# Kernel optimization log

Measured on AMD Instinct MI355X. Metric: run time of the kernel, lower is better.

The kernel has to match this reference:

```python
import jax, jax.numpy as jnp
import numpy as np

NUM_USERS = 50000
NUM_ITEMS = 50000
EMBED_DIM = 128
NUM_LAYERS = 3
NUM_EDGES = 600000
N_NODES = NUM_USERS + NUM_ITEMS


def setup_inputs() -> dict:
    key = jax.random.key(0)
    k1, k2, k3, k4, k5 = jax.random.split(key, 5)
    edge_index = jax.random.randint(k1, (2, NUM_EDGES), 0, N_NODES, dtype=jnp.int64 if jax.config.x64_enabled else jnp.int32)
    user_emb = jax.random.normal(k2, (NUM_USERS, EMBED_DIM), jnp.float32) * 0.1
    item_emb = jax.random.normal(k3, (NUM_ITEMS, EMBED_DIM), jnp.float32) * 0.1
    Wa = jax.random.normal(k4, (NUM_LAYERS, 2 * EMBED_DIM, 1), jnp.float32) * 0.05
    ba = jnp.zeros((NUM_LAYERS, 1), jnp.float32)
    Wg = jax.random.normal(k5, (NUM_LAYERS, 2 * EMBED_DIM, EMBED_DIM), jnp.float32) * 0.05
    bg = jnp.zeros((NUM_LAYERS, EMBED_DIM), jnp.float32)
    return {"edge_index": edge_index, "user_emb": user_emb, "item_emb": item_emb,
            "Wa": Wa, "ba": ba, "Wg": Wg, "bg": bg}


def reference(edge_index, user_emb, item_emb, Wa, ba, Wg, bg):
    U = user_emb.shape[0]
    N = U + item_emb.shape[0]
    src, dst = edge_index[0], edge_index[1]
    x = jnp.concatenate([user_emb, item_emb], axis=0)  # [N, d]
    for l in range(Wa.shape[0]):
        src_emb = x[src]                                # [E, d] gather
        dst_emb = x[dst]                                # [E, d] gather
        cat = jnp.concatenate([src_emb, dst_emb], 1)    # [E, 2d]
        att = jax.nn.sigmoid(cat @ Wa[l] + ba[l])       # [E, 1]
        # attention-weighted scatter-sum over destination node (zeros for isolated nodes)
        agg = jax.ops.segment_sum(src_emb * att, dst, num_segments=N)  # [N, d]
        x = jax.nn.relu(jnp.concatenate([x, agg], 1) @ Wg[l] + bg[l])  # [N, d]
    return x[:U], x[U:]
```

## Files before the change

kernel.cpp:

```cpp
#include <hip/hip_runtime.h>
#include <cstddef>
#include <cstdint>

#define NUSERS 50000
#define NITEMS 50000
#define NNODES 100000
#define DIM    128
#define NLAYERS 3
#define NEDGES 600000
#define NPAD 100096

#define EBLK  8192
#define NBLK  74
#define NBUCK 782

#define PRO_CONCAT 6250
#define PRO_WG     48
#define PRO_TOTAL  (PRO_CONCAT + PRO_WG + NBLK)

typedef __attribute__((ext_vector_type(8))) short short8;
typedef __attribute__((ext_vector_type(4))) float f32x4;

__device__ __forceinline__ float bf_lo(unsigned u) { return __uint_as_float(u << 16); }
__device__ __forceinline__ float bf_hi(unsigned u) { return __uint_as_float(u & 0xffff0000u); }
__device__ __forceinline__ unsigned short f2bf(float f) {
    unsigned b = __float_as_uint(f);
    return (unsigned short)((b + 0x7fffu + ((b >> 16) & 1u)) >> 16);
}

__device__ __forceinline__ void async16(const void* g, void* l) {
    __builtin_amdgcn_global_load_lds(
        (const __attribute__((address_space(1))) unsigned int*)(uintptr_t)g,
        (__attribute__((address_space(3))) unsigned int*)(unsigned int)(uintptr_t)l,
        16, 0, 0);
}

__global__ __launch_bounds__(256) void prologue_kernel(
        const float* __restrict__ ue, const float* __restrict__ ie,
        const float* __restrict__ Wa, const float* __restrict__ ba,
        const float* __restrict__ Wg, const int* __restrict__ dst,
        unsigned short* __restrict__ xb,
        float* __restrict__ a_src, float* __restrict__ a_dst,
        unsigned short* __restrict__ Bf, unsigned* __restrict__ counts) {
    __shared__ unsigned hist[NBUCK];
    const int blk = blockIdx.x;

    if (blk < PRO_CONCAT) {
        const int n = blk * 16 + (threadIdx.x >> 4);
        if (n >= NNODES) return;
        const int sub = threadIdx.x & 15;
        const float* r = (n < NUSERS) ? (ue + (size_t)n * DIM)
                                      : (ie + (size_t)(n - NUSERS) * DIM);
        const float4 v0 = *(const float4*)(r + sub * 8);
        const float4 v1 = *(const float4*)(r + sub * 8 + 4);
        const float4 wl0 = *(const float4*)(Wa + sub * 8);
        const float4 wl1 = *(const float4*)(Wa + sub * 8 + 4);
        const float4 wh0 = *(const float4*)(Wa + DIM + sub * 8);
        const float4 wh1 = *(const float4*)(Wa + DIM + sub * 8 + 4);

        uint4 o;
        o.x = ((unsigned)f2bf(v0.y) << 16) | (unsigned)f2bf(v0.x);
        o.y = ((unsigned)f2bf(v0.w) << 16) | (unsigned)f2bf(v0.z);
        o.z = ((unsigned)f2bf(v1.y) << 16) | (unsigned)f2bf(v1.x);
        o.w = ((unsigned)f2bf(v1.w) << 16) | (unsigned)f2bf(v1.z);
        *(uint4*)(xb + (size_t)n * DIM + sub * 8) = o;

        float ps = v0.x * wl0.x + v0.y * wl0.y + v0.z * wl0.z + v0.w * wl0.w
                 + v1.x * wl1.x + v1.y * wl1.y + v1.z * wl1.z + v1.w * wl1.w;
        float pd = v0.x * wh0.x + v0.y * wh0.y + v0.z * wh0.z + v0.w * wh0.w
                 + v1.x * wh1.x + v1.y * wh1.y + v1.z * wh1.z + v1.w * wh1.w;
        #pragma unroll
        for (int off = 1; off < 16; off <<= 1) {
            ps += __shfl_xor(ps, off);
            pd += __shfl_xor(pd, off);
        }
        if (sub == 0) { a_src[n] = ps; a_dst[n] = pd + ba[0]; }
    } else if (blk < PRO_CONCAT + PRO_WG) {
        const int tid = (blk - PRO_CONCAT) * 256 + threadIdx.x;
        if (tid >= NLAYERS * 4096) return;
        const int l    = tid >> 12;
        const int slot = tid & 4095;
        const int lane = slot & 63;
        const int t2   = slot >> 6;
        const int nf   = t2 & 3;
        const int t3   = t2 >> 2;
        const int ks   = t3 & 7;
        const int nb   = t3 >> 3;
        const int col  = nb * 64 + nf * 16 + (lane & 15);
        const int k0   = ks * 32 + (lane >> 4) * 8;
        const float* wsrc = Wg + (size_t)l * 256 * DIM;
        unsigned short o[8];
        #pragma unroll
        for (int j = 0; j < 8; ++j) o[j] = f2bf(wsrc[(size_t)(k0 + j) * DIM + col]);
        *(short8*)(Bf + (size_t)tid * 8) = *(short8*)o;
    } else {
        const int bblk = blk - PRO_CONCAT - PRO_WG;
        for (int i = threadIdx.x; i < NBUCK; i += 256) hist[i] = 0;
        __syncthreads();
        const int base = bblk * EBLK;
        const int end  = (base + EBLK < NEDGES) ? base + EBLK : NEDGES;
        for (int e = base + threadIdx.x; e < end; e += 256)
            atomicAdd(&hist[dst[e] >> 7], 1u);
        __syncthreads();
        for (int i = threadIdx.x; i < NBUCK; i += 256)
            counts[(size_t)bblk * NBUCK + i] = hist[i];
    }
}

__global__ __launch_bounds__(1024) void prefix_kernel(
        unsigned* __restrict__ counts, unsigned* __restrict__ bucketbase) {
    const int b = threadIdx.x;
    unsigned tot = 0;
    if (b < NBUCK) {
        for (int i = 0; i < NBLK; ++i) {
            const unsigned c = counts[(size_t)i * NBUCK + b];
            counts[(size_t)i * NBUCK + b] = tot;
            tot += c;
        }
    }
    const int lane = b & 63, w = b >> 6;
    unsigned s = tot;
    #pragma unroll
    for (int o = 1; o < 64; o <<= 1) {
        unsigned t = (unsigned)__shfl_up((int)s, o);
        if (lane >= o) s += t;
    }
    __shared__ unsigned wsum[16];
    if (lane == 63) wsum[w] = s;
    __syncthreads();
    unsigned add = 0;
    #pragma unroll
    for (int j = 0; j < 15; ++j) if (w > j) add += wsum[j];
    if (b < NBUCK) bucketbase[b] = s + add - tot;
    if (b == NBUCK - 1) bucketbase[NBUCK] = s + add;
}

__global__ __launch_bounds__(256) void bin_scatter_kernel(
        const int* __restrict__ src, const int* __restrict__ dst,
        const unsigned* __restrict__ counts, const unsigned* __restrict__ bucketbase,
        unsigned* __restrict__ pairs) {
    __shared__ unsigned off[NBUCK];
    for (int i = threadIdx.x; i < NBUCK; i += 256)
        off[i] = bucketbase[i] + counts[(size_t)blockIdx.x * NBUCK + i];
    __syncthreads();
    const int base = blockIdx.x * EBLK;
    const int end  = (base + EBLK < NEDGES) ? base + EBLK : NEDGES;
    for (int e = base + threadIdx.x; e < end; e += 256) {
        const int d = dst[e];
        const unsigned pos = atomicAdd(&off[d >> 7], 1u);
        pairs[pos] = ((unsigned)(d & 127) << 17) | (unsigned)src[e];
    }
}

__global__ __launch_bounds__(256) void bucket_csr_kernel(
        const unsigned* __restrict__ pairs, const unsigned* __restrict__ bucketbase,
        int* __restrict__ row_start, int* __restrict__ csr_src) {
    __shared__ unsigned deg[128], rs[128], fill[128];
    const int b = blockIdx.x;
    const unsigned seg0 = bucketbase[b], seg1 = bucketbase[b + 1];
    const int t = threadIdx.x;
    if (t < 128) deg[t] = 0;
    __syncthreads();
    for (unsigned i = seg0 + t; i < seg1; i += 256)
        atomicAdd(&deg[pairs[i] >> 17], 1u);
    __syncthreads();
    if (t < 128) rs[t] = deg[t];
    __syncthreads();
    #pragma unroll
    for (int o = 1; o < 128; o <<= 1) {
        unsigned tmp = 0;
        if (t < 128 && t >= o) tmp = rs[t - o];
        __syncthreads();
        if (t < 128) rs[t] += tmp;
        __syncthreads();
    }
    if (t < 128) {
        const unsigned excl = rs[t] - deg[t];
        fill[t] = excl;
        const int node = b * 128 + t;
        if (node < NNODES) row_start[node] = (int)(seg0 + excl);
    }
    __syncthreads();
    for (unsigned i = seg0 + t; i < seg1; i += 256) {
        const unsigned p = pairs[i];
        const unsigned r = atomicAdd(&fill[p >> 17], 1u);
        csr_src[seg0 + r] = (int)(p & 0x1ffffu);
    }
    if (b == 0 && t == 0) row_start[NNODES] = NEDGES;
}

__global__ __launch_bounds__(256) void pull_agg_kernel(
        const int* __restrict__ row_start, const int* __restrict__ csr_src,
        const float* __restrict__ a_src, const float* __restrict__ a_dst,
        const unsigned short* __restrict__ xb, unsigned short* __restrict__ aggb) {
    const int n = blockIdx.x * 16 + (threadIdx.x >> 4);
    if (n >= NNODES) return;
    const int lane = threadIdx.x & 63;
    const int sub  = lane & 15;
    const int qb   = lane & 48;
    const int beg = row_start[n], end = row_start[n + 1];
    const float adst = a_dst[n];

    float a0 = 0, a1 = 0, a2 = 0, a3 = 0, a4 = 0, a5 = 0, a6 = 0, a7 = 0;

    for (int base = beg; base < end; base += 16) {
        const int rem = end - base;
        const int cnt = rem < 16 ? rem : 16;
        int   idx_l = 0;
        float att_l = 0.0f;
        if (sub < cnt) {
            idx_l = csr_src[base + sub];
            att_l = 1.0f / (1.0f + __expf(-(a_src[idx_l] + adst)));
        }
        int i = 0;
        for (; i + 3 < cnt; i += 4) {
            const int   s0 = __shfl(idx_l, qb + i);
            const int   s1 = __shfl(idx_l, qb + i + 1);
            const int   s2 = __shfl(idx_l, qb + i + 2);
            const int   s3 = __shfl(idx_l, qb + i + 3);
            const float w0 = __shfl(att_l, qb + i);
            const float w1 = __shfl(att_l, qb + i + 1);
            const float w2 = __shfl(att_l, qb + i + 2);
            const float w3 = __shfl(att_l, qb + i + 3);
            const uint4 u0 = *(const uint4*)(xb + (size_t)s0 * DIM + sub * 8);
            const uint4 u1 = *(const uint4*)(xb + (size_t)s1 * DIM + sub * 8);
            const uint4 u2 = *(const uint4*)(xb + (size_t)s2 * DIM + sub * 8);
            const uint4 u3 = *(const uint4*)(xb + (size_t)s3 * DIM + sub * 8);
            a0 += bf_lo(u0.x) * w0 + bf_lo(u1.x) * w1 + bf_lo(u2.x) * w2 + bf_lo(u3.x) * w3;
            a1 += bf_hi(u0.x) * w0 + bf_hi(u1.x) * w1 + bf_hi(u2.x) * w2 + bf_hi(u3.x) * w3;
            a2 += bf_lo(u0.y) * w0 + bf_lo(u1.y) * w1 + bf_lo(u2.y) * w2 + bf_lo(u3.y) * w3;
            a3 += bf_hi(u0.y) * w0 + bf_hi(u1.y) * w1 + bf_hi(u2.y) * w2 + bf_hi(u3.y) * w3;
            a4 += bf_lo(u0.z) * w0 + bf_lo(u1.z) * w1 + bf_lo(u2.z) * w2 + bf_lo(u3.z) * w3;
            a5 += bf_hi(u0.z) * w0 + bf_hi(u1.z) * w1 + bf_hi(u2.z) * w2 + bf_hi(u3.z) * w3;
            a6 += bf_lo(u0.w) * w0 + bf_lo(u1.w) * w1 + bf_lo(u2.w) * w2 + bf_lo(u3.w) * w3;
            a7 += bf_hi(u0.w) * w0 + bf_hi(u1.w) * w1 + bf_hi(u2.w) * w2 + bf_hi(u3.w) * w3;
        }
        for (; i < cnt; ++i) {
            const int   s = __shfl(idx_l, qb + i);
            const float w = __shfl(att_l, qb + i);
            const uint4 u = *(const uint4*)(xb + (size_t)s * DIM + sub * 8);
            a0 += bf_lo(u.x) * w;  a1 += bf_hi(u.x) * w;
            a2 += bf_lo(u.y) * w;  a3 += bf_hi(u.y) * w;
            a4 += bf_lo(u.z) * w;  a5 += bf_hi(u.z) * w;
            a6 += bf_lo(u.w) * w;  a7 += bf_hi(u.w) * w;
        }
    }

    uint4 o;
    o.x = ((unsigned)f2bf(a1) << 16) | (unsigned)f2bf(a0);
    o.y = ((unsigned)f2bf(a3) << 16) | (unsigned)f2bf(a2);
    o.z = ((unsigned)f2bf(a5) << 16) | (unsigned)f2bf(a4);
    o.w = ((unsigned)f2bf(a7) << 16) | (unsigned)f2bf(a6);
    *(uint4*)(aggb + (size_t)n * DIM + sub * 8) = o;
}

__global__ __launch_bounds__(256, 7) void gemm_mfma_kernel(
        unsigned short* __restrict__ xb, const unsigned short* __restrict__ aggb,
        const unsigned short* __restrict__ bfr, const float* __restrict__ bg,
        const float* __restrict__ wa_next, const float* __restrict__ ba_next,
        float* __restrict__ a_src, float* __restrict__ a_dst,
        float* __restrict__ xout_f32, int write_f32, int do_dots) {
    __shared__ unsigned short At[2][32 * 128];
    __shared__ float psS[4][32], psD[4][32];

    const int tid  = threadIdx.x;
    const int lane = tid & 63;
    const int wid  = tid >> 6;
    const int mbase = blockIdx.x * 32;

    #pragma unroll
    for (int h = 0; h < 2; ++h) {
        const unsigned short* s = h ? aggb : xb;
        #pragma unroll
        for (int i = 0; i < 2; ++i) {
            const int lrow = i * 16 + wid * 4 + (lane >> 4);
            const int c    = (lane & 15) ^ (lrow & 7);
            async16(s + (size_t)(mbase + lrow) * DIM + c * 8,
                    &At[h][(i * 16 + wid * 4) * 128]);
        }
    }

    const int l16 = lane & 15, kq = lane >> 4;
    const unsigned short* bfw = bfr + (size_t)(wid >> 1) * (8 * 4 * 64 * 8);
    const int nfo = (wid & 1) * 2;

    f32x4 acc[2][2] = {};

    asm volatile("s_waitcnt vmcnt(2)" ::: "memory");
    __builtin_amdgcn_s_barrier();

    #pragma unroll
    for (int ks = 0; ks < 8; ++ks) {
        if (ks == 4) {
            asm volatile("s_waitcnt vmcnt(0)" ::: "memory");
            __builtin_amdgcn_s_barrier();
        }
        const int h = ks >> 2, ksl = ks & 3;
        short8 b[2], a[2];
        #pragma unroll
        for (int nf = 0; nf < 2; ++nf)
            b[nf] = *(const short8*)(bfw + ((size_t)(ks * 4 + nfo + nf) * 64 + lane) * 8);
        #pragma unroll
        for (int mf = 0; mf < 2; ++mf) {
            const int row   = mf * 16 + l16;
            const int chunk = (ksl * 4 + kq) ^ (row & 7);
            a[mf] = *(const short8*)&At[h][row * 128 + chunk * 8];
        }
        #pragma unroll
        for (int mf = 0; mf < 2; ++mf)
            #pragma unroll
            for (int nf = 0; nf < 2; ++nf)
                acc[mf][nf] = __builtin_amdgcn_mfma_f32_16x16x32_bf16(
                    a[mf], b[nf], acc[mf][nf], 0, 0, 0);
    }

    const int rsub = kq * 4;
    float waS[2] = {0, 0}, waD[2] = {0, 0}, bias[2];
    #pragma unroll
    for (int nf = 0; nf < 2; ++nf) {
        const int col = wid * 32 + nf * 16 + l16;
        bias[nf] = bg[col];
        if (do_dots) { waS[nf] = wa_next[col]; waD[nf] = wa_next[DIM + col]; }
    }
    #pragma unroll
    for (int mf = 0; mf < 2; ++mf) {
        #pragma unroll
        for (int j = 0; j < 4; ++j) {
            const int row = mbase + mf * 16 + rsub + j;
            float s = 0.0f, d = 0.0f;
            #pragma unroll
            for (int nf = 0; nf < 2; ++nf) {
                const int col = wid * 32 + nf * 16 + l16;
                const float v = fmaxf(acc[mf][nf][j] + bias[nf], 0.0f);
                if (write_f32) {
                    xout_f32[(size_t)row * DIM + col] = v;
                } else {
                    const unsigned short bv = f2bf(v);
                    const unsigned pb = (unsigned)(unsigned short)__shfl_xor((int)bv, 1);
                    if (!(l16 & 1))
                        *(unsigned*)(xb + (size_t)row * DIM + col) =
                            (unsigned)bv | (pb << 16);
                }
                s += v * waS[nf];
                d += v * waD[nf];
            }
            if (do_dots) {
                #pragma unroll
                for (int off = 1; off < 16; off <<= 1) {
                    s += __shfl_xor(s, off);
                    d += __shfl_xor(d, off);
                }
                if (l16 == 0) {
                    const int rl = mf * 16 + rsub + j;
                    psS[wid][rl] = s;
                    psD[wid][rl] = d;
                }
            }
        }
    }
    if (do_dots) {
        __syncthreads();
        if (tid < 32) {
            const int row = mbase + tid;
            a_src[row] = psS[0][tid] + psS[1][tid] + psS[2][tid] + psS[3][tid];
            a_dst[row] = psD[0][tid] + psD[1][tid] + psD[2][tid] + psD[3][tid]
                       + ba_next[0];
        }
    }
}

extern "C" void kernel_launch(void* const* d_in, const int* in_sizes, int n_in,
                              void* d_out, int out_size, void* d_ws, size_t ws_size,
                              hipStream_t stream) {
    const int*   edge = (const int*)d_in[0];
    const float* ue   = (const float*)d_in[1];
    const float* ie   = (const float*)d_in[2];
    const float* Wa   = (const float*)d_in[3];
    const float* ba   = (const float*)d_in[4];
    const float* Wg   = (const float*)d_in[5];
    const float* bg   = (const float*)d_in[6];

    const int* src = edge;
    const int* dst = edge + NEDGES;

    float* x = (float*)d_out;

    unsigned short* xb   = (unsigned short*)d_ws;
    unsigned short* aggb = xb + (size_t)NPAD * DIM;
    unsigned short* bfr  = aggb + (size_t)NPAD * DIM;
    float* a_src      = (float*)(bfr + NLAYERS * 32768);
    float* a_dst      = a_src + NPAD;
    int*   row_start  = (int*)(a_dst + NPAD);
    int*   csr_src    = row_start + NPAD + 256;
    unsigned* pairs   = (unsigned*)(csr_src + NEDGES);
    unsigned* counts  = pairs + NEDGES;
    unsigned* bbase   = counts + (size_t)NBLK * NBUCK;

    prologue_kernel<<<PRO_TOTAL, 256, 0, stream>>>(
        ue, ie, Wa, ba, Wg, dst, xb, a_src, a_dst, bfr, counts);

    prefix_kernel<<<1, 1024, 0, stream>>>(counts, bbase);
    bin_scatter_kernel<<<NBLK, 256, 0, stream>>>(src, dst, counts, bbase, pairs);
    bucket_csr_kernel<<<NBUCK, 256, 0, stream>>>(pairs, bbase, row_start, csr_src);

    const int gemm_blocks = NNODES / 32;
    const int pull_blocks = (NNODES + 15) / 16;
    for (int l = 0; l < NLAYERS; ++l) {
        pull_agg_kernel<<<pull_blocks, 256, 0, stream>>>(
            row_start, csr_src, a_src, a_dst, xb, aggb);
        const int last = (l == NLAYERS - 1);
        gemm_mfma_kernel<<<gemm_blocks, 256, 0, stream>>>(
            xb, aggb, bfr + (size_t)l * 32768, bg + (size_t)l * DIM,
            Wa + (size_t)(l + 1 < NLAYERS ? l + 1 : 0) * 256,
            ba + (l + 1 < NLAYERS ? l + 1 : 0),
            a_src, a_dst, x, last ? 1 : 0, last ? 0 : 1);
    }
}
```

Baseline: 222.8 us.

## Use 8 lanes per node in pull aggregation and transpose bucket counts

The pull aggregation kernel now assigns 8 lanes per destination node, each handling 16 features with two 16-byte loads, so each wave covers 8 nodes and processes neighbor chunks of 8. The aim is to cut idle lanes on low-degree nodes (average degree is about 6) and raise memory-level parallelism. The per-block bucket counts are stored transposed with padding, so the prefix scan reads contiguous rows. The bucket CSR scan switches from a shared-memory Hillis-Steele loop with many barriers to wave shuffles. The per-thread register footprint of the pull kernel grows, and the bounds check is dropped because 100000 divides evenly by 32.

Result: slower. 261.5 us (+17.3%).

```diff
diff --git a/kernel.cpp b/kernel.cpp
--- a/kernel.cpp
+++ b/kernel.cpp
@@ -12,6 +12,7 @@
 
 #define EBLK  8192
 #define NBLK  74
+#define NBLKP 76
 #define NBUCK 782
 
 #define PRO_CONCAT 6250
@@ -26,6 +27,9 @@
 __device__ __forceinline__ unsigned short f2bf(float f) {
     unsigned b = __float_as_uint(f);
     return (unsigned short)((b + 0x7fffu + ((b >> 16) & 1u)) >> 16);
+}
+__device__ __forceinline__ unsigned pack2(float lo, float hi) {
+    return ((unsigned)f2bf(hi) << 16) | (unsigned)f2bf(lo);
 }
 
 __device__ __forceinline__ void async16(const void* g, void* l) {
@@ -59,10 +63,10 @@
         const float4 wh1 = *(const float4*)(Wa + DIM + sub * 8 + 4);
 
         uint4 o;
-        o.x = ((unsigned)f2bf(v0.y) << 16) | (unsigned)f2bf(v0.x);
-        o.y = ((unsigned)f2bf(v0.w) << 16) | (unsigned)f2bf(v0.z);
-        o.z = ((unsigned)f2bf(v1.y) << 16) | (unsigned)f2bf(v1.x);
-        o.w = ((unsigned)f2bf(v1.w) << 16) | (unsigned)f2bf(v1.z);
+        o.x = pack2(v0.x, v0.y);
+        o.y = pack2(v0.z, v0.w);
+        o.z = pack2(v1.x, v1.y);
+        o.w = pack2(v1.z, v1.w);
         *(uint4*)(xb + (size_t)n * DIM + sub * 8) = o;
 
         float ps = v0.x * wl0.x + v0.y * wl0.y + v0.z * wl0.z + v0.w * wl0.w
@@ -103,7 +107,7 @@
             atomicAdd(&hist[dst[e] >> 7], 1u);
         __syncthreads();
         for (int i = threadIdx.x; i < NBUCK; i += 256)
-            counts[(size_t)bblk * NBUCK + i] = hist[i];
+            counts[(size_t)i * NBLKP + bblk] = hist[i];
     }
 }
 
@@ -112,9 +116,11 @@
     const int b = threadIdx.x;
     unsigned tot = 0;
     if (b < NBUCK) {
+        unsigned* row = counts + (size_t)b * NBLKP;
+        #pragma unroll 8
         for (int i = 0; i < NBLK; ++i) {
-            const unsigned c = counts[(size_t)i * NBUCK + b];
-            counts[(size_t)i * NBUCK + b] = tot;
+            const unsigned c = row[i];
+            row[i] = tot;
             tot += c;
         }
     }
@@ -141,7 +147,7 @@
         unsigned* __restrict__ pairs) {
     __shared__ unsigned off[NBUCK];
     for (int i = threadIdx.x; i < NBUCK; i += 256)
-        off[i] = bucketbase[i] + counts[(size_t)blockIdx.x * NBUCK + i];
+        off[i] = bucketbase[i] + counts[(size_t)i * NBLKP + blockIdx.x];
     __syncthreads();
     const int base = blockIdx.x * EBLK;
     const int end  = (base + EBLK < NEDGES) ? base + EBLK : NEDGES;
@@ -155,7 +161,7 @@
 __global__ __launch_bounds__(256) void bucket_csr_kernel(
         const unsigned* __restrict__ pairs, const unsigned* __restrict__ bucketbase,
         int* __restrict__ row_start, int* __restrict__ csr_src) {
-    __shared__ unsigned deg[128], rs[128], fill[128];
+    __shared__ unsigned deg[128], fill[128], wtot[2];
     const int b = blockIdx.x;
     const unsigned seg0 = bucketbase[b], seg1 = bucketbase[b + 1];
     const int t = threadIdx.x;
@@ -164,18 +170,22 @@
     for (unsigned i = seg0 + t; i < seg1; i += 256)
         atomicAdd(&deg[pairs[i] >> 17], 1u);
     __syncthreads();
-    if (t < 128) rs[t] = deg[t];
-    __syncthreads();
-    #pragma unroll
-    for (int o = 1; o < 128; o <<= 1) {
-        unsigned tmp = 0;
-        if (t < 128 && t >= o) tmp = rs[t - o];
-        __syncthreads();
-        if (t < 128) rs[t] += tmp;
-        __syncthreads();
-    }
+    unsigned incl = 0, v = 0;
     if (t < 128) {
-        const unsigned excl = rs[t] - deg[t];
+        v = deg[t];
+        unsigned s = v;
+        #pragma unroll
+        for (int o = 1; o < 64; o <<= 1) {
+            const unsigned tmp = (unsigned)__shfl_up((int)s, o);
+            if ((t & 63) >= o) s += tmp;
+        }
+        if ((t & 63) == 63) wtot[t >> 6] = s;
+        incl = s;
+    }
+    __syncthreads();
+    if (t < 128) {
+        if (t >= 64) incl += wtot[0];
+        const unsigned excl = incl - v;
         fill[t] = excl;
         const int node = b * 128 + t;
         if (node < NNODES) row_start[node] = (int)(seg0 + excl);
@@ -193,19 +203,19 @@
         const int* __restrict__ row_start, const int* __restrict__ csr_src,
         const float* __restrict__ a_src, const float* __restrict__ a_dst,
         const unsigned short* __restrict__ xb, unsigned short* __restrict__ aggb) {
-    const int n = blockIdx.x * 16 + (threadIdx.x >> 4);
-    if (n >= NNODES) return;
+    const int n = blockIdx.x * 32 + (threadIdx.x >> 3);
     const int lane = threadIdx.x & 63;
-    const int sub  = lane & 15;
-    const int qb   = lane & 48;
+    const int sub  = lane & 7;
+    const int qb   = lane & 56;
     const int beg = row_start[n], end = row_start[n + 1];
     const float adst = a_dst[n];
 
     float a0 = 0, a1 = 0, a2 = 0, a3 = 0, a4 = 0, a5 = 0, a6 = 0, a7 = 0;
-
-    for (int base = beg; base < end; base += 16) {
+    float b0 = 0, b1 = 0, b2 = 0, b3 = 0, b4 = 0, b5 = 0, b6 = 0, b7 = 0;
+
+    for (int base = beg; base < end; base += 8) {
         const int rem = end - base;
-        const int cnt = rem < 16 ? rem : 16;
+        const int cnt = rem < 8 ? rem : 8;
         int   idx_l = 0;
         float att_l = 0.0f;
         if (sub < cnt) {
@@ -214,44 +224,56 @@
         }
         int i = 0;
         for (; i + 3 < cnt; i += 4) {
-            const int   s0 = __shfl(idx_l, qb + i);
-            const int   s1 = __shfl(idx_l, qb + i + 1);
-            const int   s2 = __shfl(idx_l, qb + i + 2);
-            const int   s3 = __shfl(idx_l, qb + i + 3);
-            const float w0 = __shfl(att_l, qb + i);
-            const float w1 = __shfl(att_l, qb + i + 1);
-            const float w2 = __shfl(att_l, qb + i + 2);
-            const float w3 = __shfl(att_l, qb + i + 3);
-            const uint4 u0 = *(const uint4*)(xb + (size_t)s0 * DIM + sub * 8);
-            const uint4 u1 = *(const uint4*)(xb + (size_t)s1 * DIM + sub * 8);
-            const uint4 u2 = *(const uint4*)(xb + (size_t)s2 * DIM + sub * 8);
-            const uint4 u3 = *(const uint4*)(xb + (size_t)s3 * DIM + sub * 8);
-            a0 += bf_lo(u0.x) * w0 + bf_lo(u1.x) * w1 + bf_lo(u2.x) * w2 + bf_lo(u3.x) * w3;
-            a1 += bf_hi(u0.x) * w0 + bf_hi(u1.x) * w1 + bf_hi(u2.x) * w2 + bf_hi(u3.x) * w3;
-            a2 += bf_lo(u0.y) * w0 + bf_lo(u1.y) * w1 + bf_lo(u2.y) * w2 + bf_lo(u3.y) * w3;
-            a3 += bf_hi(u0.y) * w0 + bf_hi(u1.y) * w1 + bf_hi(u2.y) * w2 + bf_hi(u3.y) * w3;
-            a4 += bf_lo(u0.z) * w0 + bf_lo(u1.z) * w1 + bf_lo(u2.z) * w2 + bf_lo(u3.z) * w3;
-            a5 += bf_hi(u0.z) * w0 + bf_hi(u1.z) * w1 + bf_hi(u2.z) * w2 + bf_hi(u3.z) * w3;
-            a6 += bf_lo(u0.w) * w0 + bf_lo(u1.w) * w1 + bf_lo(u2.w) * w2 + bf_lo(u3.w) * w3;
-            a7 += bf_hi(u0.w) * w0 + bf_hi(u1.w) * w1 + bf_hi(u2.w) * w2 + bf_hi(u3.w) * w3;
+            int s[4]; float w[4];
+            #pragma unroll
+            for (int k = 0; k < 4; ++k) {
+                s[k] = __shfl(idx_l, qb + i + k);
+                w[k] = __shfl(att_l, qb + i + k);
+            }
+            uint4 ua[4], ub[4];
+            #pragma unroll
+            for (int k = 0; k < 4; ++k) {
+                const unsigned short* rp = xb + (size_t)s[k] * DIM + sub * 16;
+                ua[k] = *(const uint4*)rp;
+                ub[k] = *(const uint4*)(rp + 8);
+            }
+            #pragma unroll
+            for (int k = 0; k < 4; ++k) {
+                a0 += bf_lo(ua[k].x) * w[k];  a1 += bf_hi(ua[k].x) * w[k];
+                a2 += bf_lo(ua[k].y) * w[k];  a3 += bf_hi(ua[k].y) * w[k];
+                a4 += bf_lo(ua[k].z) * w[k];  a5 += bf_hi(ua[k].z) * w[k];
+                a6 += bf_lo(ua[k].w) * w[k];  a7 += bf_hi(ua[k].w) * w[k];
+                b0 += bf_lo(ub[k].x) * w[k];  b1 += bf_hi(ub[k].x) * w[k];
+                b2 += bf_lo(ub[k].y) * w[k];  b3 += bf_hi(ub[k].y) * w[k];
+                b4 += bf_lo(ub[k].z) * w[k];  b5 += bf_hi(ub[k].z) * w[k];
+                b6 += bf_lo(ub[k].w) * w[k];  b7 += bf_hi(ub[k].w) * w[k];
+            }
         }
         for (; i < cnt; ++i) {
             const int   s = __shfl(idx_l, qb + i);
             const float w = __shfl(att_l, qb + i);
-            const uint4 u = *(const uint4*)(xb + (size_t)s * DIM + sub * 8);
-            a0 += bf_lo(u.x) * w;  a1 += bf_hi(u.x) * w;
-            a2 += bf_lo(u.y) * w;  a3 += bf_hi(u.y) * w;
-            a4 += bf_lo(u.z) * w;  a5 += bf_hi(u.z) * w;
-            a6 += bf_lo(u.w) * w;  a7 += bf_hi(u.w) * w;
-        }
-    }
-
+            const unsigned short* rp = xb + (size_t)s * DIM + sub * 16;
+            const uint4 ua = *(const uint4*)rp;
+            const uint4 ub = *(const uint4*)(rp + 8);
+            a0 += bf_lo(ua.x) * w;  a1 += bf_hi(ua.x) * w;
+            a2 += bf_lo(ua.y) * w;  a3 += bf_hi(ua.y) * w;
+            a4 += bf_lo(ua.z) * w;  a5 += bf_hi(ua.z) * w;
+            a6 += bf_lo(ua.w) * w;  a7 += bf_hi(ua.w) * w;
+            b0 += bf_lo(ub.x) * w;  b1 += bf_hi(ub.x) * w;
+            b2 += bf_lo(ub.y) * w;  b3 += bf_hi(ub.y) * w;
+            b4 += bf_lo(ub.z) * w;  b5 += bf_hi(ub.z) * w;
+            b6 += bf_lo(ub.w) * w;  b7 += bf_hi(ub.w) * w;
+        }
+    }
+
+    unsigned short* op = aggb + (size_t)n * DIM + sub * 16;
     uint4 o;
-    o.x = ((unsigned)f2bf(a1) << 16) | (unsigned)f2bf(a0);
-    o.y = ((unsigned)f2bf(a3) << 16) | (unsigned)f2bf(a2);
-    o.z = ((unsigned)f2bf(a5) << 16) | (unsigned)f2bf(a4);
-    o.w = ((unsigned)f2bf(a7) << 16) | (unsigned)f2bf(a6);
-    *(uint4*)(aggb + (size_t)n * DIM + sub * 8) = o;
+    o.x = pack2(a0, a1); o.y = pack2(a2, a3);
+    o.z = pack2(a4, a5); o.w = pack2(a6, a7);
+    *(uint4*)op = o;
+    o.x = pack2(b0, b1); o.y = pack2(b2, b3);
+    o.z = pack2(b4, b5); o.w = pack2(b6, b7);
+    *(uint4*)(op + 8) = o;
 }
 
 __global__ __launch_bounds__(256, 7) void gemm_mfma_kernel(
@@ -394,7 +416,7 @@
     int*   csr_src    = row_start + NPAD + 256;
     unsigned* pairs   = (unsigned*)(csr_src + NEDGES);
     unsigned* counts  = pairs + NEDGES;
-    unsigned* bbase   = counts + (size_t)NBLK * NBUCK;
+    unsigned* bbase   = counts + (size_t)NBUCK * NBLKP;
 
     prologue_kernel<<<PRO_TOTAL, 256, 0, stream>>>(
         ue, ie, Wa, ba, Wg, dst, xb, a_src, a_dst, bfr, counts);
@@ -404,7 +426,7 @@
     bucket_csr_kernel<<<NBUCK, 256, 0, stream>>>(pairs, bbase, row_start, csr_src);
 
     const int gemm_blocks = NNODES / 32;
-    const int pull_blocks = (NNODES + 15) / 16;
+    const int pull_blocks = NNODES / 32;
     for (int l = 0; l < NLAYERS; ++l) {
         pull_agg_kernel<<<pull_blocks, 256, 0, stream>>>(
             row_start, csr_src, a_src, a_dst, xb, aggb);
```
